# Kernel optimization log

Measured on AMD Instinct MI355X. Metric: run time of the kernel, lower is better.

The kernel has to match this reference:

```python
import jax, jax.numpy as jnp
import numpy as np

B, N, H = 8, 256, 128  # graphs, nodes per graph (equal counts), hidden_dim


def setup_inputs() -> dict:
    key = jax.random.key(0)
    k1, k2, k3, k4, k5, k6 = jax.random.split(key, 6)
    total = B * N
    h = jax.random.normal(k1, (total, H), dtype=jnp.float32)
    pos = jax.random.normal(k2, (total, 3), dtype=jnp.float32)
    # sorted segment ids, equal counts per graph (padding becomes a reshape)
    batch = jnp.repeat(jnp.arange(B, dtype=jnp.int64), N)
    # phi: Linear(2H+1 -> H) -> SiLU -> Linear(H -> 1), torch default init
    s1 = 1.0 / np.sqrt(2 * H + 1)
    s2 = 1.0 / np.sqrt(H)
    W1 = jax.random.uniform(k3, (2 * H + 1, H), minval=-s1, maxval=s1, dtype=jnp.float32)
    b1 = jax.random.uniform(k4, (H,), minval=-s1, maxval=s1, dtype=jnp.float32)
    W2 = jax.random.uniform(k5, (H, 1), minval=-s2, maxval=s2, dtype=jnp.float32)
    b2 = jax.random.uniform(k6, (1,), minval=-s2, maxval=s2, dtype=jnp.float32)
    return {"h": h, "pos": pos, "batch": batch, "W1": W1, "b1": b1, "W2": W2, "b2": b2}


def _safe_norm(diff):
    # exact forward (0 on diagonal), grad-safe (no nan from sqrt at 0)
    sq = jnp.sum(diff * diff, axis=-1, keepdims=True)
    pos_sq = sq > 0
    return jnp.where(pos_sq, jnp.sqrt(jnp.where(pos_sq, sq, 1.0)), 0.0)


def reference(h, pos, batch, W1, b1, W2, b2):
    # batch is sorted with equal counts per graph -> padding == reshape,
    # mask is all-True, so v_pred_padded[mask] == reshape back to [total, 3].
    hp = h.reshape(B, N, H)
    pp = pos.reshape(B, N, 3)

    # diff[b, p, q] = pos[b, q] - pos[b, p]  (matches unsqueeze(1) - unsqueeze(2))
    diff = pp[:, None, :, :] - pp[:, :, None, :]        # [B, N, N, 3]
    dist = _safe_norm(diff)                              # [B, N, N, 1]

    # cat([h_i, h_j, dist]) @ W1 done without materializing the concat:
    # h_i[b,p,q] = h[b,q], h_j[b,p,q] = h[b,p]
    Wa, Wb, wd = W1[:H], W1[H:2 * H], W1[2 * H]
    pre = (hp @ Wa)[:, None, :, :] + (hp @ Wb)[:, :, None, :] + dist * wd + b1
    coeff = jax.nn.silu(pre) @ W2 + b2                   # [B, N, N, 1]

    v = jnp.sum(coeff * diff, axis=2)                    # [B, N, 3]
    return v.reshape(B * N, 3)
```

## Files before the change

### kernel.cpp

```cpp
#include <hip/hip_runtime.h>
#include <math.h>

#define BATCH 8
#define NPTS  256
#define HDIM  128
#define TOTAL (BATCH * NPTS)
#define PRE_SCALE 0.25f

__global__ __launch_bounds__(HDIM) void evh_prep_kernel(
    const float* __restrict__ h, const float* __restrict__ W1,
    const float* __restrict__ b1, const float* __restrict__ W2,
    const float* __restrict__ pos,
    float* __restrict__ A_T4, float4* __restrict__ U,
    float4* __restrict__ pos4,
    float* __restrict__ lamA, float* __restrict__ lamB,
    float* __restrict__ lamD, float* __restrict__ out)
{
    __shared__ float hrow[HDIM];
    __shared__ float sA[2], sB[2], sD[2];
    const int t = blockIdx.x;
    const int c = threadIdx.x;
    const int wv = c >> 6, ln = c & 63;
    hrow[c] = h[t * HDIM + c];
    const float w2c = W2[c];
    const float wdc = W1[2 * HDIM * HDIM + c];
    if (c < 3) out[t * 3 + c] = 0.f;
    if (c == 0)
        pos4[t] = make_float4(pos[t * 3], pos[t * 3 + 1], pos[t * 3 + 2], 0.f);
    __syncthreads();

    float a = 0.f, bsum = 0.f;
#pragma unroll 8
    for (int k = 0; k < HDIM; ++k) {
        const float hv = hrow[k];
        a    = fmaf(hv, W1[k * HDIM + c], a);
        bsum = fmaf(hv, W1[(HDIM + k) * HDIM + c], bsum);
    }
    const float bb = bsum + b1[c];
    A_T4[(c >> 2) * (4 * TOTAL) + 4 * t + (c & 3)] = a * PRE_SCALE;

    float* up = reinterpret_cast<float*>(&U[(size_t)(t >> 1) * HDIM + c]);
    up[t & 1] = bb * PRE_SCALE;
    if ((t & 1) == 0) { up[2] = wdc * PRE_SCALE; up[3] = w2c; }

    float va = w2c * a, vb = w2c * bb;
#pragma unroll
    for (int off = 32; off >= 1; off >>= 1) {
        va += __shfl_xor(va, off, 64);
        vb += __shfl_xor(vb, off, 64);
    }
    if (ln == 0) { sA[wv] = va; sB[wv] = vb; }
    __syncthreads();
    if (c == 0) {
        lamA[t] = 0.5f * (sA[0] + sA[1]);
        lamB[t] = 0.5f * (sB[0] + sB[1]);
    }

    if (t == 0) {
        float vd = w2c * wdc;
#pragma unroll
        for (int off = 32; off >= 1; off >>= 1) vd += __shfl_xor(vd, off, 64);
        if (ln == 0) sD[wv] = vd;
        __syncthreads();
        if (c == 0) lamD[0] = 0.5f * (sD[0] + sD[1]);
    }
}

__global__ __launch_bounds__(256, 8) void evh_pair_kernel(
    const float* __restrict__ A_T4, const float4* __restrict__ U,
    const float4* __restrict__ pos4,
    const float* __restrict__ lamA, const float* __restrict__ lamB,
    const float* __restrict__ lamD, const float* __restrict__ b2,
    float* __restrict__ out,
    float q0, float q1, float q2, float q3, float q4, float q5, float q6)
{
    const int blk = blockIdx.x;
    const int ch  = blk & 1;
    const int b   = blk >> 8;
    const int ipl = (blk >> 1) & 127;
    const int i0  = ipl * 2;
    const int tid = threadIdx.x;
    const int brow  = b * NPTS;
    const int row_j = brow + tid;

    const float4 pj = pos4[row_j];
    const float4 pi0 = pos4[brow + i0];
    const float4 pi1 = pos4[brow + i0 + 1];
    const float dx0 = pj.x - pi0.x, dy0 = pj.y - pi0.y, dz0 = pj.z - pi0.z;
    const float dx1 = pj.x - pi1.x, dy1 = pj.y - pi1.y, dz1 = pj.z - pi1.z;
    const float dist0 = sqrtf(dx0 * dx0 + dy0 * dy0 + dz0 * dz0);
    const float dist1 = sqrtf(dx1 * dx1 + dy1 * dy1 + dz1 * dz1);

    const float4* __restrict__ up = U + (size_t)(b * 128 + ipl) * HDIM + ch * 64;
    const float* __restrict__ ap  = A_T4 + 4 * row_j
                                    + (size_t)(ch * 16) * (4 * TOTAL);

    float acc0 = 0.f, acc1 = 0.f;

#define CELL(AK, UQ)                                                    \
    {                                                                   \
        const float t0 = fmaf(dist0, (UQ).z, (AK) + (UQ).x);            \
        const float t1 = fmaf(dist1, (UQ).z, (AK) + (UQ).y);            \
        const float y0 = fmaf(t0, t0, -1.0f);                           \
        const float y1 = fmaf(t1, t1, -1.0f);                           \
        float r0 = fmaf(q6, y0, q5), r1 = fmaf(q6, y1, q5);             \
        r0 = fmaf(r0, y0, q4);  r1 = fmaf(r1, y1, q4);                  \
        r0 = fmaf(r0, y0, q3);  r1 = fmaf(r1, y1, q3);                  \
        r0 = fmaf(r0, y0, q2);  r1 = fmaf(r1, y1, q2);                  \
        r0 = fmaf(r0, y0, q1);  r1 = fmaf(r1, y1, q1);                  \
        r0 = fmaf(r0, y0, q0);  r1 = fmaf(r1, y1, q0);                  \
        acc0 = fmaf((UQ).w, r0, acc0);                                  \
        acc1 = fmaf((UQ).w, r1, acc1);                                  \
    }

#pragma unroll 4
    for (int q = 0; q < 16; ++q) {
        const float4 a  = *reinterpret_cast<const float4*>(
                              ap + (size_t)q * (4 * TOTAL));
        const float4 u0 = up[4 * q + 0];
        const float4 u1 = up[4 * q + 1];
        const float4 u2 = up[4 * q + 2];
        const float4 u3 = up[4 * q + 3];

        CELL(a.x, u0)
        CELL(a.y, u1)
        CELL(a.z, u2)
        CELL(a.w, u3)
    }
#undef CELL

    float c0 = acc0, c1 = acc1;
    if (ch == 0) {
        const float la = lamA[row_j];
        const float ld = lamD[0];
        const float bv = b2[0];
        c0 += la + lamB[brow + i0]     + dist0 * ld + bv;
        c1 += la + lamB[brow + i0 + 1] + dist1 * ld + bv;
    }

    const int wave = tid >> 6;
    const int lane = tid & 63;
    float v0x = c0 * dx0, v0y = c0 * dy0, v0z = c0 * dz0;
    float v1x = c1 * dx1, v1y = c1 * dy1, v1z = c1 * dz1;
#pragma unroll
    for (int off = 32; off >= 1; off >>= 1) {
        v0x += __shfl_xor(v0x, off, 64);
        v0y += __shfl_xor(v0y, off, 64);
        v0z += __shfl_xor(v0z, off, 64);
        v1x += __shfl_xor(v1x, off, 64);
        v1y += __shfl_xor(v1y, off, 64);
        v1z += __shfl_xor(v1z, off, 64);
    }

    __shared__ float vsh[4][6];
    if (lane == 0) {
        vsh[wave][0] = v0x; vsh[wave][1] = v0y; vsh[wave][2] = v0z;
        vsh[wave][3] = v1x; vsh[wave][4] = v1y; vsh[wave][5] = v1z;
    }
    __syncthreads();
    if (tid < 6) {
        const float val = vsh[0][tid] + vsh[1][tid] + vsh[2][tid] + vsh[3][tid];
        const int s = tid / 3, comp = tid % 3;
        atomicAdd(&out[(brow + i0 + s) * 3 + comp], val);
    }
}

extern "C" void kernel_launch(void* const* d_in, const int* in_sizes, int n_in,
                              void* d_out, int out_size, void* d_ws, size_t ws_size,
                              hipStream_t stream) {
    const float* h   = (const float*)d_in[0];
    const float* pos = (const float*)d_in[1];
    const float* W1  = (const float*)d_in[3];
    const float* b1  = (const float*)d_in[4];
    const float* W2  = (const float*)d_in[5];
    const float* b2  = (const float*)d_in[6];
    float* out = (float*)d_out;

    float4* U    = (float4*)d_ws;
    float*  A_T4 = (float*)(U + (size_t)(TOTAL / 2) * HDIM);
    float4* pos4 = (float4*)(A_T4 + (size_t)TOTAL * HDIM);
    float*  lamA = (float*)(pos4 + TOTAL);
    float*  lamB = lamA + TOTAL;
    float*  lamD = lamB + TOTAL;

    const double PI = 3.14159265358979323846;
    double cc[7] = {0, 0, 0, 0, 0, 0, 0};
    const int M = 64;
    for (int m = 0; m < M; ++m) {
        const double th = PI * (m + 0.5) / M;
        const double yp = cos(th);
        const double s  = 16.0 * (1.0 + yp);
        const double x  = sqrt(s > 0 ? s : 0);
        const double f  = 0.5 * x * tanh(0.5 * x);
        for (int k = 0; k < 7; ++k) cc[k] += f * cos(k * th);
    }
    for (int k = 0; k < 7; ++k) cc[k] *= 2.0 / M;
    cc[0] *= 0.5;
    const double p0 = cc[0] - cc[2] + cc[4] - cc[6];
    const double p1 = cc[1] - 3 * cc[3] + 5 * cc[5];
    const double p2 = 2 * cc[2] - 8 * cc[4] + 18 * cc[6];
    const double p3 = 4 * cc[3] - 20 * cc[5];
    const double p4 = 8 * cc[4] - 48 * cc[6];
    const double p5 = 16 * cc[5];
    const double p6 = 32 * cc[6];

    evh_prep_kernel<<<TOTAL, HDIM, 0, stream>>>(h, W1, b1, W2, pos,
                                                A_T4, U, pos4,
                                                lamA, lamB, lamD, out);
    evh_pair_kernel<<<TOTAL, 256, 0, stream>>>(A_T4, U, pos4,
                                               lamA, lamB, lamD, b2, out,
                                               (float)p0, (float)p1, (float)p2,
                                               (float)p3, (float)p4, (float)p5,
                                               (float)p6);
}
```

Measured before the change: 34.01 us.

## Recast pairwise SiLU sum as polynomial-expanded bf16 MFMA GEMM

Replaces the per-pair polynomial evaluation of the SiLU term with a separable polynomial expansion in the two node features and a Taylor expansion in distance. The pairwise sum over hidden channels becomes a batched bf16 GEMM with K=128*11 on MFMA units, followed by a combine kernel that applies distance powers and reduces to the output vectors. This trades per-pair scalar FMAs for matrix-core throughput. In exchange it adds a large bf16 feature expansion in the prep kernel, a third launch, an fp32 intermediate X, and accuracy risk from bf16 rounding and a truncated degree-10 polynomial.

```diff
diff --git a/kernel.cpp b/kernel.cpp
--- a/kernel.cpp
+++ b/kernel.cpp
@@ -1,4 +1,5 @@
 #include <hip/hip_runtime.h>
+#include <hip/hip_bf16.h>
 #include <math.h>
 
 #define BATCH 8
@@ -6,21 +7,31 @@
 #define HDIM  128
 #define TOTAL (BATCH * NPTS)
 #define PRE_SCALE 0.25f
+#define DEG   10
+#define NQ    11
+#define KDIM  (HDIM * NQ)
+#define MROWS (3 * NPTS)
+
+typedef __attribute__((ext_vector_type(8))) short short8;
+typedef __attribute__((ext_vector_type(4))) float f32x4;
+
+struct QC { float v[3][NQ][NQ]; };
 
 __global__ __launch_bounds__(HDIM) void evh_prep_kernel(
     const float* __restrict__ h, const float* __restrict__ W1,
     const float* __restrict__ b1, const float* __restrict__ W2,
     const float* __restrict__ pos,
-    float* __restrict__ A_T4, float4* __restrict__ U,
+    __hip_bfloat16* __restrict__ Uf, __hip_bfloat16* __restrict__ Vf,
     float4* __restrict__ pos4,
     float* __restrict__ lamA, float* __restrict__ lamB,
-    float* __restrict__ lamD, float* __restrict__ out)
+    float* __restrict__ lamD, float* __restrict__ out, QC qc)
 {
     __shared__ float hrow[HDIM];
     __shared__ float sA[2], sB[2], sD[2];
     const int t = blockIdx.x;
     const int c = threadIdx.x;
     const int wv = c >> 6, ln = c & 63;
+    const int b = t >> 8, jj = t & 255;
     hrow[c] = h[t * HDIM + c];
     const float w2c = W2[c];
     const float wdc = W1[2 * HDIM * HDIM + c];
@@ -37,11 +48,27 @@
         bsum = fmaf(hv, W1[(HDIM + k) * HDIM + c], bsum);
     }
     const float bb = bsum + b1[c];
-    A_T4[(c >> 2) * (4 * TOTAL) + 4 * t + (c & 3)] = a * PRE_SCALE;
-
-    float* up = reinterpret_cast<float*>(&U[(size_t)(t >> 1) * HDIM + c]);
-    up[t & 1] = bb * PRE_SCALE;
-    if ((t & 1) == 0) { up[2] = wdc * PRE_SCALE; up[3] = w2c; }
+
+    const float u = a * PRE_SCALE;
+    const float v = bb * PRE_SCALE;
+    const float w = wdc * PRE_SCALE;
+    const float alph[3] = { w2c, w2c * w, 0.5f * w2c * w * w };
+    for (int n = 0; n < 3; ++n) {
+        __hip_bfloat16* dst =
+            Uf + ((size_t)((b * 3 + n) * NPTS + jj)) * KDIM + c * NQ;
+        const float an = alph[n];
+        for (int q = 0; q < NQ; ++q) {
+            const int dp = DEG - q;
+            float r = qc.v[n][q][dp];
+            for (int p = dp - 1; p >= 0; --p) r = fmaf(r, u, qc.v[n][q][p]);
+            dst[q] = __float2bfloat16(an * r);
+        }
+    }
+    {
+        __hip_bfloat16* vdst = Vf + ((size_t)(b * NPTS + jj)) * KDIM + c * NQ;
+        float vp = 1.f;
+        for (int q = 0; q < NQ; ++q) { vdst[q] = __float2bfloat16(vp); vp *= v; }
+    }
 
     float va = w2c * a, vb = w2c * bb;
 #pragma unroll
@@ -55,7 +82,6 @@
         lamA[t] = 0.5f * (sA[0] + sA[1]);
         lamB[t] = 0.5f * (sB[0] + sB[1]);
     }
-
     if (t == 0) {
         float vd = w2c * wdc;
 #pragma unroll
@@ -66,80 +92,103 @@
     }
 }
 
-__global__ __launch_bounds__(256, 8) void evh_pair_kernel(
-    const float* __restrict__ A_T4, const float4* __restrict__ U,
-    const float4* __restrict__ pos4,
+__global__ __launch_bounds__(256) void evh_gemm_kernel(
+    const __hip_bfloat16* __restrict__ Uf, const __hip_bfloat16* __restrict__ Vf,
+    float* __restrict__ X)
+{
+    const int blk = blockIdx.x;
+    const int b    = blk & 7;
+    const int tile = blk >> 3;
+    const int tm   = tile % 12;
+    const int tn   = tile / 12;
+    const int tid  = threadIdx.x;
+    const int wave = tid >> 6, lane = tid & 63;
+    const int mrow = lane & 15, kb = lane >> 4;
+
+    const int m0 = tm * 64 + (wave >> 1) * 32;
+    const int n0 = tn * 64 + (wave & 1) * 32;
+
+    const __hip_bfloat16* __restrict__ Ub = Uf + (size_t)b * MROWS * KDIM;
+    const __hip_bfloat16* __restrict__ Vb = Vf + (size_t)b * NPTS * KDIM;
+
+    f32x4 acc[2][2] = {};
+
+#define LDA(MM, KO) (*reinterpret_cast<const short8*>(Ub + (size_t)(MM) * KDIM + (KO)))
+#define LDB(NN, KO) (*reinterpret_cast<const short8*>(Vb + (size_t)(NN) * KDIM + (KO)))
+
+    int koff = kb * 8;
+    short8 A0 = LDA(m0 + mrow, koff),      A1 = LDA(m0 + 16 + mrow, koff);
+    short8 B0 = LDB(n0 + mrow, koff),      B1 = LDB(n0 + 16 + mrow, koff);
+
+    for (int kk = 0; kk < KDIM / 32; ++kk) {
+        short8 nA0, nA1, nB0, nB1;
+        if (kk + 1 < KDIM / 32) {
+            const int nk = (kk + 1) * 32 + kb * 8;
+            nA0 = LDA(m0 + mrow, nk);      nA1 = LDA(m0 + 16 + mrow, nk);
+            nB0 = LDB(n0 + mrow, nk);      nB1 = LDB(n0 + 16 + mrow, nk);
+        }
+        acc[0][0] = __builtin_amdgcn_mfma_f32_16x16x32_bf16(A0, B0, acc[0][0], 0, 0, 0);
+        acc[0][1] = __builtin_amdgcn_mfma_f32_16x16x32_bf16(A0, B1, acc[0][1], 0, 0, 0);
+        acc[1][0] = __builtin_amdgcn_mfma_f32_16x16x32_bf16(A1, B0, acc[1][0], 0, 0, 0);
+        acc[1][1] = __builtin_amdgcn_mfma_f32_16x16x32_bf16(A1, B1, acc[1][1], 0, 0, 0);
+        A0 = nA0; A1 = nA1; B0 = nB0; B1 = nB1;
+    }
+#undef LDA
+#undef LDB
+
+#pragma unroll
+    for (int fm = 0; fm < 2; ++fm) {
+#pragma unroll
+        for (int fn = 0; fn < 2; ++fn) {
+            const int mbase = m0 + fm * 16 + (lane >> 4) * 4;
+            const int i     = n0 + fn * 16 + (lane & 15);
+            const int nfeat = mbase >> 8;
+            const int j0    = mbase & 255;
+            float* dst = X + ((size_t)((b * 3 + nfeat) * NPTS + i)) * NPTS + j0;
+            *reinterpret_cast<float4*>(dst) =
+                *reinterpret_cast<float4*>(&acc[fm][fn]);
+        }
+    }
+}
+
+__global__ __launch_bounds__(256) void evh_comb_kernel(
+    const float* __restrict__ X, const float4* __restrict__ pos4,
     const float* __restrict__ lamA, const float* __restrict__ lamB,
     const float* __restrict__ lamD, const float* __restrict__ b2,
-    float* __restrict__ out,
-    float q0, float q1, float q2, float q3, float q4, float q5, float q6)
+    float* __restrict__ out)
 {
     const int blk = blockIdx.x;
-    const int ch  = blk & 1;
-    const int b   = blk >> 8;
-    const int ipl = (blk >> 1) & 127;
-    const int i0  = ipl * 2;
+    const int b   = blk >> 7;
+    const int i0  = (blk & 127) * 2;
     const int tid = threadIdx.x;
-    const int brow  = b * NPTS;
+    const int brow = b * NPTS;
     const int row_j = brow + tid;
 
-    const float4 pj = pos4[row_j];
+    const float4 pj  = pos4[row_j];
     const float4 pi0 = pos4[brow + i0];
     const float4 pi1 = pos4[brow + i0 + 1];
     const float dx0 = pj.x - pi0.x, dy0 = pj.y - pi0.y, dz0 = pj.z - pi0.z;
     const float dx1 = pj.x - pi1.x, dy1 = pj.y - pi1.y, dz1 = pj.z - pi1.z;
-    const float dist0 = sqrtf(dx0 * dx0 + dy0 * dy0 + dz0 * dz0);
-    const float dist1 = sqrtf(dx1 * dx1 + dy1 * dy1 + dz1 * dz1);
-
-    const float4* __restrict__ up = U + (size_t)(b * 128 + ipl) * HDIM + ch * 64;
-    const float* __restrict__ ap  = A_T4 + 4 * row_j
-                                    + (size_t)(ch * 16) * (4 * TOTAL);
-
-    float acc0 = 0.f, acc1 = 0.f;
-
-#define CELL(AK, UQ)                                                    \
-    {                                                                   \
-        const float t0 = fmaf(dist0, (UQ).z, (AK) + (UQ).x);            \
-        const float t1 = fmaf(dist1, (UQ).z, (AK) + (UQ).y);            \
-        const float y0 = fmaf(t0, t0, -1.0f);                           \
-        const float y1 = fmaf(t1, t1, -1.0f);                           \
-        float r0 = fmaf(q6, y0, q5), r1 = fmaf(q6, y1, q5);             \
-        r0 = fmaf(r0, y0, q4);  r1 = fmaf(r1, y1, q4);                  \
-        r0 = fmaf(r0, y0, q3);  r1 = fmaf(r1, y1, q3);                  \
-        r0 = fmaf(r0, y0, q2);  r1 = fmaf(r1, y1, q2);                  \
-        r0 = fmaf(r0, y0, q1);  r1 = fmaf(r1, y1, q1);                  \
-        r0 = fmaf(r0, y0, q0);  r1 = fmaf(r1, y1, q0);                  \
-        acc0 = fmaf((UQ).w, r0, acc0);                                  \
-        acc1 = fmaf((UQ).w, r1, acc1);                                  \
-    }
-
-#pragma unroll 4
-    for (int q = 0; q < 16; ++q) {
-        const float4 a  = *reinterpret_cast<const float4*>(
-                              ap + (size_t)q * (4 * TOTAL));
-        const float4 u0 = up[4 * q + 0];
-        const float4 u1 = up[4 * q + 1];
-        const float4 u2 = up[4 * q + 2];
-        const float4 u3 = up[4 * q + 3];
-
-        CELL(a.x, u0)
-        CELL(a.y, u1)
-        CELL(a.z, u2)
-        CELL(a.w, u3)
-    }
-#undef CELL
-
-    float c0 = acc0, c1 = acc1;
-    if (ch == 0) {
-        const float la = lamA[row_j];
-        const float ld = lamD[0];
-        const float bv = b2[0];
-        c0 += la + lamB[brow + i0]     + dist0 * ld + bv;
-        c1 += la + lamB[brow + i0 + 1] + dist1 * ld + bv;
-    }
-
-    const int wave = tid >> 6;
-    const int lane = tid & 63;
+    const float d0 = sqrtf(dx0 * dx0 + dy0 * dy0 + dz0 * dz0);
+    const float d1 = sqrtf(dx1 * dx1 + dy1 * dy1 + dz1 * dz1);
+
+    const size_t xb = (size_t)(b * 3) * NPTS * NPTS;
+    const float x00 = X[xb + (size_t)(0 * NPTS + i0)     * NPTS + tid];
+    const float x01 = X[xb + (size_t)(0 * NPTS + i0 + 1) * NPTS + tid];
+    const float x10 = X[xb + (size_t)(1 * NPTS + i0)     * NPTS + tid];
+    const float x11 = X[xb + (size_t)(1 * NPTS + i0 + 1) * NPTS + tid];
+    const float x20 = X[xb + (size_t)(2 * NPTS + i0)     * NPTS + tid];
+    const float x21 = X[xb + (size_t)(2 * NPTS + i0 + 1) * NPTS + tid];
+
+    const float la = lamA[row_j];
+    const float ld = lamD[0];
+    const float bv = b2[0];
+    const float c0 = la + lamB[brow + i0]     + d0 * ld + bv
+                     + x00 + d0 * x10 + d0 * d0 * x20;
+    const float c1 = la + lamB[brow + i0 + 1] + d1 * ld + bv
+                     + x01 + d1 * x11 + d1 * d1 * x21;
+
+    const int wave = tid >> 6, lane = tid & 63;
     float v0x = c0 * dx0, v0y = c0 * dy0, v0z = c0 * dz0;
     float v1x = c1 * dx1, v1y = c1 * dy1, v1z = c1 * dz1;
 #pragma unroll
@@ -151,7 +200,6 @@
         v1y += __shfl_xor(v1y, off, 64);
         v1z += __shfl_xor(v1z, off, 64);
     }
-
     __shared__ float vsh[4][6];
     if (lane == 0) {
         vsh[wave][0] = v0x; vsh[wave][1] = v0y; vsh[wave][2] = v0z;
@@ -176,40 +224,65 @@
     const float* b2  = (const float*)d_in[6];
     float* out = (float*)d_out;
 
-    float4* U    = (float4*)d_ws;
-    float*  A_T4 = (float*)(U + (size_t)(TOTAL / 2) * HDIM);
-    float4* pos4 = (float4*)(A_T4 + (size_t)TOTAL * HDIM);
-    float*  lamA = (float*)(pos4 + TOTAL);
-    float*  lamB = lamA + TOTAL;
-    float*  lamD = lamB + TOTAL;
+    float* X = (float*)d_ws;
+    float4* pos4 = (float4*)(X + (size_t)BATCH * 3 * NPTS * NPTS);
+    float* lamA = (float*)(pos4 + TOTAL);
+    float* lamB = lamA + TOTAL;
+    float* lamD = lamB + TOTAL;
+    __hip_bfloat16* Uf = (__hip_bfloat16*)(lamD + 4);
+    __hip_bfloat16* Vf = Uf + (size_t)BATCH * MROWS * KDIM;
 
     const double PI = 3.14159265358979323846;
-    double cc[7] = {0, 0, 0, 0, 0, 0, 0};
-    const int M = 64;
+    const double T = 1.30;
+    double cc[DEG + 1] = {0};
+    const int M = 128;
     for (int m = 0; m < M; ++m) {
         const double th = PI * (m + 0.5) / M;
-        const double yp = cos(th);
-        const double s  = 16.0 * (1.0 + yp);
-        const double x  = sqrt(s > 0 ? s : 0);
-        const double f  = 0.5 * x * tanh(0.5 * x);
-        for (int k = 0; k < 7; ++k) cc[k] += f * cos(k * th);
-    }
-    for (int k = 0; k < 7; ++k) cc[k] *= 2.0 / M;
+        const double z = cos(th);
+        const double tau = T * z;
+        const double g = 2.0 * tau * tanh(2.0 * tau);
+        for (int k = 0; k <= DEG; ++k) cc[k] += g * cos(k * th);
+    }
+    for (int k = 0; k <= DEG; ++k) cc[k] *= 2.0 / M;
     cc[0] *= 0.5;
-    const double p0 = cc[0] - cc[2] + cc[4] - cc[6];
-    const double p1 = cc[1] - 3 * cc[3] + 5 * cc[5];
-    const double p2 = 2 * cc[2] - 8 * cc[4] + 18 * cc[6];
-    const double p3 = 4 * cc[3] - 20 * cc[5];
-    const double p4 = 8 * cc[4] - 48 * cc[6];
-    const double p5 = 16 * cc[5];
-    const double p6 = 32 * cc[6];
+    double Tm[DEG + 1][DEG + 1] = {{0}};
+    Tm[0][0] = 1; Tm[1][1] = 1;
+    for (int k = 2; k <= DEG; ++k)
+        for (int p = 0; p <= k; ++p)
+            Tm[k][p] = 2.0 * (p > 0 ? Tm[k - 1][p - 1] : 0.0) - Tm[k - 2][p];
+    double e[DEG + 1] = {0};
+    {
+        double tp = 1.0;
+        for (int p = 0; p <= DEG; ++p) {
+            double s = 0;
+            for (int k = 0; k <= DEG; ++k) s += cc[k] * Tm[k][p];
+            e[p] = s / tp;
+            tp *= T;
+        }
+    }
+    for (int p = 1; p <= DEG; p += 2) e[p] = 0.0;
+    double P[3][DEG + 1] = {{0}};
+    for (int p = 0; p <= DEG; ++p) P[0][p] = e[p];
+    for (int p = 0; p <= DEG - 1; ++p) P[1][p] = (p + 1) * e[p + 1];
+    for (int p = 0; p <= DEG - 2; ++p) P[2][p] = 0.5 * (p + 2) * (p + 1) * e[p + 2];
+    for (int p = 0; p <= DEG - 2; ++p) P[2][p] = (p + 2) * (p + 1) * e[p + 2];
+    double C[NQ][NQ] = {{0}};
+    for (int n = 0; n < NQ; ++n) {
+        C[n][0] = 1;
+        for (int k = 1; k <= n; ++k)
+            C[n][k] = C[n - 1][k - 1] + (k <= n - 1 ? C[n - 1][k] : 0.0);
+    }
+    QC qc;
+    for (int n = 0; n < 3; ++n)
+        for (int q = 0; q < NQ; ++q)
+            for (int p = 0; p < NQ; ++p)
+                qc.v[n][q][p] =
+                    (p + q <= DEG) ? (float)(P[n][p + q] * C[p + q][p]) : 0.f;
 
     evh_prep_kernel<<<TOTAL, HDIM, 0, stream>>>(h, W1, b1, W2, pos,
-                                                A_T4, U, pos4,
-                                                lamA, lamB, lamD, out);
-    evh_pair_kernel<<<TOTAL, 256, 0, stream>>>(A_T4, U, pos4,
-                                               lamA, lamB, lamD, b2, out,
-                                               (float)p0, (float)p1, (float)p2,
-                                               (float)p3, (float)p4, (float)p5,
-                                               (float)p6);
-}
+                                                Uf, Vf, pos4,
+                                                lamA, lamB, lamD, out, qc);
+    evh_gemm_kernel<<<48 * BATCH, 256, 0, stream>>>(Uf, Vf, X);
+    evh_comb_kernel<<<BATCH * (NPTS / 2), 256, 0, stream>>>(
+        X, pos4, lamA, lamB, lamD, b2, out);
+}
```

After: 74.79 us. +119.9%, slower.
